# Optimization experiments

Hardware: AMD Instinct MI355X
Metric: run time of the kernel (lower is better)

## Reference

```python
import jax, jax.numpy as jnp
import numpy as np

EPS = 1e-12  # matches torch F.normalize eps


def setup_inputs() -> dict:
    key = jax.random.key(0)
    k1, k2, k3 = jax.random.split(key, 3)
    V, F = 2048, 4096
    vertices = jax.random.normal(k1, (V, 3), dtype=jnp.float32)
    faces = jax.random.randint(k2, (F, 3), 0, V, dtype=jnp.int64)
    face_probs = jax.random.uniform(k3, (F,), dtype=jnp.float32)
    return {"vertices": vertices, "faces": faces, "face_probs": face_probs}


def reference(vertices, faces, face_probs):
    F_ = faces.shape[0]
    tri = vertices[faces]                      # [F,3,3] gathered triangle vertices
    v1 = tri[:, 1] - tri[:, 0]
    v2 = tri[:, 2] - tri[:, 0]
    n = jnp.cross(v1, v2)
    n = n / jnp.maximum(jnp.linalg.norm(n, axis=1, keepdims=True), EPS)  # [F,3]

    centroids = tri.mean(axis=1)               # [F,3]
    # squared distances; dist < 1.0 <=> dist^2 < 1.0
    d2 = jnp.sum((centroids[:, None, :] - centroids[None, :, :]) ** 2, axis=-1)  # [F,F]
    nearby = (d2 < 1.0) & ~jnp.eye(F_, dtype=bool)

    # signed distance of each vertex of triangle j to the plane of triangle i:
    # S[i,j,k] = (tri[j,k] - tri[i,0]) . n[i]
    ref_dot = jnp.einsum('id,id->i', tri[:, 0], n)          # [F]
    S = jnp.einsum('jkd,id->ijk', tri, n) - ref_dot[:, None, None]  # [F,F,3]

    rolled = jnp.roll(S, 1, axis=2)
    intersections = jnp.any(S * rolled < 0, axis=2)          # [F,F]

    collision_count = jnp.sum(nearby & intersections, axis=1).astype(face_probs.dtype)  # [F]
    return jnp.mean(face_probs * collision_count)
```

## Files before the change

### kernel.cpp

```cpp
#include <hip/hip_runtime.h>

#define FF 4096
#define IC 32
#define BJ 256
#define NBX (FF / BJ)
#define NBY (FF / IC)
#define NPART (NBX * NBY)

#define WS_NJ 0
#define WS_CP (WS_NJ + FF)
#define WS_TV (WS_CP + FF)
#define WS_PART (WS_TV + 3 * FF)

__global__ __launch_bounds__(256) void tcl_pre(
    const float* __restrict__ verts,
    const int* __restrict__ faces,
    const float* __restrict__ probs,
    float4* __restrict__ ws)
{
    int f = blockIdx.x * blockDim.x + threadIdx.x;
    if (f >= FF) return;

    int a = faces[3 * f + 0];
    int b = faces[3 * f + 1];
    int c = faces[3 * f + 2];
    float p0x = verts[3 * a], p0y = verts[3 * a + 1], p0z = verts[3 * a + 2];
    float p1x = verts[3 * b], p1y = verts[3 * b + 1], p1z = verts[3 * b + 2];
    float p2x = verts[3 * c], p2y = verts[3 * c + 1], p2z = verts[3 * c + 2];

    float v1x = p1x - p0x, v1y = p1y - p0y, v1z = p1z - p0z;
    float v2x = p2x - p0x, v2y = p2y - p0y, v2z = p2z - p0z;
    float nx = v1y * v2z - v1z * v2y;
    float ny = v1z * v2x - v1x * v2z;
    float nz = v1x * v2y - v1y * v2x;
    float nrm = sqrtf(nx * nx + ny * ny + nz * nz);
    float inv = 1.0f / fmaxf(nrm, 1e-12f);
    nx *= inv; ny *= inv; nz *= inv;
    float rd = p0x * nx + p0y * ny + p0z * nz;

    ws[WS_NJ + f] = make_float4(nx, ny, nz, rd);
    ws[WS_CP + f] = make_float4((p0x + p1x + p2x) * (1.0f / 3.0f),
                                (p0y + p1y + p2y) * (1.0f / 3.0f),
                                (p0z + p1z + p2z) * (1.0f / 3.0f),
                                probs[f]);
    ws[WS_TV + 3 * f + 0] = make_float4(p0x, p0y, p0z, 0.0f);
    ws[WS_TV + 3 * f + 1] = make_float4(p1x, p1y, p1z, 0.0f);
    ws[WS_TV + 3 * f + 2] = make_float4(p2x, p2y, p2z, 0.0f);
}

__global__ __launch_bounds__(256) void tcl_pairs(
    const float4* __restrict__ ws,
    float* __restrict__ partial)
{
    __shared__ float4 s_n[IC];
    __shared__ float4 s_cp[IC];
    __shared__ float s_red[4];

    const int tid = threadIdx.x;
    const int j = blockIdx.x * BJ + tid;
    const int ibase = blockIdx.y * IC;

    float4 t0 = ws[WS_TV + 3 * j + 0];
    float4 t1 = ws[WS_TV + 3 * j + 1];
    float4 t2 = ws[WS_TV + 3 * j + 2];
    float4 cj = ws[WS_CP + j];

    if (tid < IC) {
        s_n[tid]  = ws[WS_NJ + ibase + tid];
        s_cp[tid] = ws[WS_CP + ibase + tid];
    }
    __syncthreads();

    float acc = 0.0f;
    #pragma unroll 8
    for (int ii = 0; ii < IC; ++ii) {
        float4 nf = s_n[ii];
        float4 cp = s_cp[ii];

        float dx = cp.x - cj.x;
        float dy = cp.y - cj.y;
        float dz = cp.z - cj.z;
        float d2 = fmaf(dx, dx, fmaf(dy, dy, dz * dz));

        float S0 = fmaf(t0.x, nf.x, fmaf(t0.y, nf.y, fmaf(t0.z, nf.z, -nf.w)));
        float S1 = fmaf(t1.x, nf.x, fmaf(t1.y, nf.y, fmaf(t1.z, nf.z, -nf.w)));
        float S2 = fmaf(t2.x, nf.x, fmaf(t2.y, nf.y, fmaf(t2.z, nf.z, -nf.w)));

        float mn = fminf(fminf(S0, S1), S2);
        float mx = fmaxf(fmaxf(S0, S1), S2);

        bool ok = (mn * mx < 0.0f) & (d2 < 1.0f) & (ibase + ii != j);
        acc += ok ? cp.w : 0.0f;
    }

    #pragma unroll
    for (int off = 32; off > 0; off >>= 1)
        acc += __shfl_down(acc, off, 64);

    int wave = tid >> 6;
    int lane = tid & 63;
    if (lane == 0) s_red[wave] = acc;
    __syncthreads();
    if (tid == 0)
        partial[blockIdx.y * NBX + blockIdx.x] =
            s_red[0] + s_red[1] + s_red[2] + s_red[3];
}

__global__ __launch_bounds__(512) void tcl_reduce(
    const float4* __restrict__ partial4,
    float* __restrict__ d_out)
{
    __shared__ float s_red[8];
    int tid = threadIdx.x;
    float4 v = partial4[tid];
    float s = (v.x + v.y) + (v.z + v.w);

    #pragma unroll
    for (int off = 32; off > 0; off >>= 1)
        s += __shfl_down(s, off, 64);

    int wave = tid >> 6;
    int lane = tid & 63;
    if (lane == 0) s_red[wave] = s;
    __syncthreads();
    if (tid == 0) {
        float t = 0.0f;
        #pragma unroll
        for (int k = 0; k < 8; ++k) t += s_red[k];
        d_out[0] = t * (1.0f / (float)FF);
    }
}

extern "C" void kernel_launch(void* const* d_in, const int* in_sizes, int n_in,
                              void* d_out, int out_size, void* d_ws, size_t ws_size,
                              hipStream_t stream)
{
    const float* verts = (const float*)d_in[0];
    const int* faces   = (const int*)d_in[1];
    const float* probs = (const float*)d_in[2];
    float* out = (float*)d_out;

    float4* ws = (float4*)d_ws;
    float* partial = (float*)(ws + WS_PART);

    tcl_pre<<<FF / 256, 256, 0, stream>>>(verts, faces, probs, ws);

    dim3 grid(NBX, NBY);
    tcl_pairs<<<grid, BJ, 0, stream>>>(ws, partial);

    tcl_reduce<<<1, 512, 0, stream>>>((const float4*)partial, out);
}
```

Measured before the change: 20.24 us.

## Register-block four j faces per thread in pair kernel to reuse shared i data

```diff
diff --git a/kernel.cpp b/kernel.cpp
--- a/kernel.cpp
+++ b/kernel.cpp
@@ -1,8 +1,10 @@
 #include <hip/hip_runtime.h>
 
 #define FF 4096
-#define IC 32
-#define BJ 256
+#define IC 16
+#define JR 4
+#define BJT 256
+#define BJ (BJT * JR)
 #define NBX (FF / BJ)
 #define NBY (FF / IC)
 #define NPART (NBX * NBY)
@@ -48,7 +50,7 @@
     ws[WS_TV + 3 * f + 2] = make_float4(p2x, p2y, p2z, 0.0f);
 }
 
-__global__ __launch_bounds__(256) void tcl_pairs(
+__global__ __launch_bounds__(256, 4) void tcl_pairs(
     const float4* __restrict__ ws,
     float* __restrict__ partial)
 {
@@ -57,13 +59,18 @@
     __shared__ float s_red[4];
 
     const int tid = threadIdx.x;
-    const int j = blockIdx.x * BJ + tid;
+    const int jbase = blockIdx.x * BJ + tid;
     const int ibase = blockIdx.y * IC;
 
-    float4 t0 = ws[WS_TV + 3 * j + 0];
-    float4 t1 = ws[WS_TV + 3 * j + 1];
-    float4 t2 = ws[WS_TV + 3 * j + 2];
-    float4 cj = ws[WS_CP + j];
+    float4 T0[JR], T1[JR], T2[JR], CJ[JR];
+    #pragma unroll
+    for (int k = 0; k < JR; ++k) {
+        int j = jbase + k * BJT;
+        T0[k] = ws[WS_TV + 3 * j + 0];
+        T1[k] = ws[WS_TV + 3 * j + 1];
+        T2[k] = ws[WS_TV + 3 * j + 2];
+        CJ[k] = ws[WS_CP + j];
+    }
 
     if (tid < IC) {
         s_n[tid]  = ws[WS_NJ + ibase + tid];
@@ -71,26 +78,31 @@
     }
     __syncthreads();
 
+    const int d0 = ibase - jbase;
+
     float acc = 0.0f;
-    #pragma unroll 8
+    #pragma unroll 4
     for (int ii = 0; ii < IC; ++ii) {
         float4 nf = s_n[ii];
         float4 cp = s_cp[ii];
 
-        float dx = cp.x - cj.x;
-        float dy = cp.y - cj.y;
-        float dz = cp.z - cj.z;
-        float d2 = fmaf(dx, dx, fmaf(dy, dy, dz * dz));
+        #pragma unroll
+        for (int k = 0; k < JR; ++k) {
+            float dx = cp.x - CJ[k].x;
+            float dy = cp.y - CJ[k].y;
+            float dz = cp.z - CJ[k].z;
+            float d2 = fmaf(dx, dx, fmaf(dy, dy, dz * dz));
 
-        float S0 = fmaf(t0.x, nf.x, fmaf(t0.y, nf.y, fmaf(t0.z, nf.z, -nf.w)));
-        float S1 = fmaf(t1.x, nf.x, fmaf(t1.y, nf.y, fmaf(t1.z, nf.z, -nf.w)));
-        float S2 = fmaf(t2.x, nf.x, fmaf(t2.y, nf.y, fmaf(t2.z, nf.z, -nf.w)));
+            float S0 = fmaf(T0[k].x, nf.x, fmaf(T0[k].y, nf.y, fmaf(T0[k].z, nf.z, -nf.w)));
+            float S1 = fmaf(T1[k].x, nf.x, fmaf(T1[k].y, nf.y, fmaf(T1[k].z, nf.z, -nf.w)));
+            float S2 = fmaf(T2[k].x, nf.x, fmaf(T2[k].y, nf.y, fmaf(T2[k].z, nf.z, -nf.w)));
 
-        float mn = fminf(fminf(S0, S1), S2);
-        float mx = fmaxf(fmaxf(S0, S1), S2);
+            float mn = fminf(fminf(S0, S1), S2);
+            float mx = fmaxf(fmaxf(S0, S1), S2);
 
-        bool ok = (mn * mx < 0.0f) & (d2 < 1.0f) & (ibase + ii != j);
-        acc += ok ? cp.w : 0.0f;
+            bool ok = (mn * mx < 0.0f) & (d2 < 1.0f) & (d0 + ii != k * BJT);
+            acc += ok ? cp.w : 0.0f;
+        }
     }
 
     #pragma unroll
@@ -106,11 +118,11 @@
             s_red[0] + s_red[1] + s_red[2] + s_red[3];
 }
 
-__global__ __launch_bounds__(512) void tcl_reduce(
+__global__ __launch_bounds__(256) void tcl_reduce(
     const float4* __restrict__ partial4,
     float* __restrict__ d_out)
 {
-    __shared__ float s_red[8];
+    __shared__ float s_red[4];
     int tid = threadIdx.x;
     float4 v = partial4[tid];
     float s = (v.x + v.y) + (v.z + v.w);
@@ -124,9 +136,7 @@
     if (lane == 0) s_red[wave] = s;
     __syncthreads();
     if (tid == 0) {
-        float t = 0.0f;
-        #pragma unroll
-        for (int k = 0; k < 8; ++k) t += s_red[k];
+        float t = (s_red[0] + s_red[1]) + (s_red[2] + s_red[3]);
         d_out[0] = t * (1.0f / (float)FF);
     }
 }
@@ -146,7 +156,7 @@
     tcl_pre<<<FF / 256, 256, 0, stream>>>(verts, faces, probs, ws);
 
     dim3 grid(NBX, NBY);
-    tcl_pairs<<<grid, BJ, 0, stream>>>(ws, partial);
+    tcl_pairs<<<grid, BJT, 0, stream>>>(ws, partial);
 
-    tcl_reduce<<<1, 512, 0, stream>>>((const float4*)partial, out);
+    tcl_reduce<<<1, 256, 0, stream>>>((const float4*)partial, out);
 }
```

New measurement: 21.88 us. 8.1% more time.
